# Kernel tuning notes

Measured on AMD Instinct MI355X. Metric: run time of the kernel, lower is better.

Reference implementation:

```python
import jax, jax.numpy as jnp
import numpy as np

N_HEAD = 16
COND_LEN = 256  # n_unmasked; mask[i, j] == 1 iff j < COND_LEN + i


def rotate_half(x):
    # interleaved pairs: (x0, x1, x2, x3, ...) -> (-x1, x0, -x3, x2, ...)
    x = x.reshape(x.shape[:-1] + (-1, 2))
    x1, x2 = x[..., 0], x[..., 1]
    return jnp.stack([-x2, x1], axis=-1).reshape(x.shape[:-2] + (-1,))


def apply_rotary_pos_emb(t, freqs):
    # t: [B, H, T, l], freqs: [T, l] -> broadcast over B, H
    return t * jnp.cos(freqs) + rotate_half(t) * jnp.sin(freqs)


def setup_inputs() -> dict:
    key = jax.random.key(0)
    ks = jax.random.split(key, 12)
    B, T, C = 8, 769, 1024
    l = 32
    s = 0.02
    return {
        "x_q": jax.random.normal(ks[0], (B, T, C), jnp.float32),
        "x_kv": jax.random.normal(ks[1], (B, T, C), jnp.float32),
        "rotary_pos_emb": jax.random.uniform(ks[2], (T, l), jnp.float32),
        "Wq": jax.random.normal(ks[3], (C, C), jnp.float32) * s,
        "bq": jnp.zeros((C,), jnp.float32),
        "Wk": jax.random.normal(ks[4], (C, C), jnp.float32) * s,
        "bk": jnp.zeros((C,), jnp.float32),
        "Wv": jax.random.normal(ks[5], (C, C), jnp.float32) * s,
        "bv": jnp.zeros((C,), jnp.float32),
        "Wp": jax.random.normal(ks[6], (C, C), jnp.float32) * s,
        "bp": jnp.zeros((C,), jnp.float32),
    }


def reference(x_q, x_kv, rotary_pos_emb, Wq, bq, Wk, bk, Wv, bv, Wp, bp):
    B, T_q, C = x_q.shape
    T_kv = x_kv.shape[1]
    H = N_HEAD
    hd = C // H

    def heads(x, W, b, T):
        return (x @ W.T + b).reshape(B, T, H, hd).transpose(0, 2, 1, 3)  # [B,H,T,hd]

    q = heads(x_q, Wq, bq, T_q)
    k = heads(x_kv, Wk, bk, T_kv)
    v = heads(x_kv, Wv, bv, T_kv)

    # partial rotary on first l dims of q and k
    l = rotary_pos_emb.shape[-1]
    q = jnp.concatenate([apply_rotary_pos_emb(q[..., :l], rotary_pos_emb), q[..., l:]], axis=-1)
    k = jnp.concatenate([apply_rotary_pos_emb(k[..., :l], rotary_pos_emb), k[..., l:]], axis=-1)

    att = jnp.einsum("bhqd,bhkd->bhqk", q, k) * (1.0 / jnp.sqrt(jnp.asarray(hd, q.dtype)))
    # custom prefix+causal mask: allowed iff col < COND_LEN + row
    row = jnp.arange(T_q)[:, None]
    col = jnp.arange(T_kv)[None, :]
    allowed = col < (COND_LEN + row)  # [T_q, T_kv]
    att = jnp.where(allowed[None, None], att, -jnp.inf)
    att = jax.nn.softmax(att, axis=-1)

    y = jnp.einsum("bhqk,bhkd->bhqd", att, v)
    y = y.transpose(0, 2, 1, 3).reshape(B, T_q, C)
    return y @ Wp.T + bp
```

## Files before the change

### kernel.cpp

```cpp
#include <hip/hip_runtime.h>
#include <stdint.h>

#define B_    8
#define T_    769
#define C_    1024
#define H_    16
#define COND_ 256
#define NTOK  (B_*T_)
#define BH_   (B_*H_)
#define TP_   896

typedef short    v8s  __attribute__((ext_vector_type(8)));
typedef float    v4f  __attribute__((ext_vector_type(4)));
typedef uint16_t u16x4 __attribute__((ext_vector_type(4)));
typedef uint16_t u16x8 __attribute__((ext_vector_type(8)));

__device__ __forceinline__ uint16_t f2bf(float f) {
  uint32_t u = __builtin_bit_cast(uint32_t, f);
  u += 0x7fffu + ((u >> 16) & 1u);
  return (uint16_t)(u >> 16);
}
__device__ __forceinline__ float bf2f(uint16_t h) {
  uint32_t u = ((uint32_t)h) << 16;
  return __builtin_bit_cast(float, u);
}

__device__ __forceinline__ void gl_lds16(const void* gptr, void* lptr) {
  __builtin_amdgcn_global_load_lds(
      (const __attribute__((address_space(1))) uint32_t*)gptr,
      (__attribute__((address_space(3))) uint32_t*)lptr,
      16, 0, 0);
}

__global__ __launch_bounds__(256) void convert_bf16(
    const float* xq, const float* xkv, const float* wq, const float* wk,
    const float* wv, const float* wp,
    uint16_t* dxq, uint16_t* dxkv, uint16_t* dwq, uint16_t* dwk,
    uint16_t* dwv, uint16_t* dwp)
{
  int bid = blockIdx.x;
  const float* s; uint16_t* d; int base;
  if (bid < 6152)       { s = xq;  d = dxq;  base = bid; }
  else if (bid < 12304) { s = xkv; d = dxkv; base = bid - 6152; }
  else {
    int r = bid - 12304;
    int wsel = r >> 10; base = r & 1023;
    s = (wsel == 0) ? wq : (wsel == 1) ? wk : (wsel == 2) ? wv : wp;
    d = (wsel == 0) ? dwq : (wsel == 1) ? dwk : (wsel == 2) ? dwv : dwp;
  }
  int i = base * 256 + threadIdx.x;
  float4 f = ((const float4*)s)[i];
  u16x4 o;
  o[0] = f2bf(f.x); o[1] = f2bf(f.y); o[2] = f2bf(f.z); o[3] = f2bf(f.w);
  ((u16x4*)d)[i] = o;
}

__device__ __forceinline__ void gemm_mainloop64(
    const uint16_t* A, const uint16_t* W, int M, int row0, int col0,
    v4f acc[4][4], uint16_t* sA, uint16_t* sB)
{
  const int tid = threadIdx.x;
  const int lane = tid & 63, w = tid >> 6, quad = lane >> 4, l15 = lane & 15;
  const int rbase = (w >> 1) * 64, cbase = (w & 1) * 64;

  const uint16_t* Aptr[4];
  const uint16_t* Bptr[4];
  #pragma unroll
  for (int r = 0; r < 4; r++) {
    int c = r * 256 + tid;
    int row = c >> 3, qp = c & 7;
    int g = qp ^ (row & 7);
    Aptr[r] = A + (size_t)min(row0 + row, M - 1) * 1024 + g * 8;
    Bptr[r] = W + (size_t)(col0 + row) * 1024 + g * 8;
  }

  #pragma unroll
  for (int i = 0; i < 4; i++)
    #pragma unroll
    for (int j = 0; j < 4; j++) acc[i][j] = (v4f)0.0f;

  for (int k0 = 0; k0 < 1024; k0 += 64) {
    #pragma unroll
    for (int r = 0; r < 4; r++) {
      gl_lds16(Aptr[r] + k0, sA + (r * 256 + tid) * 8);
      gl_lds16(Bptr[r] + k0, sB + (r * 256 + tid) * 8);
    }
    __syncthreads();
    #pragma unroll
    for (int s = 0; s < 2; s++) {
      v8s af[4], bf[4];
      #pragma unroll
      for (int i = 0; i < 4; i++) {
        int m = rbase + i * 16 + l15;
        af[i] = *(const v8s*)(sA + m * 64 + (((s * 4 + quad) ^ (m & 7)) * 8));
      }
      #pragma unroll
      for (int j = 0; j < 4; j++) {
        int n = cbase + j * 16 + l15;
        bf[j] = *(const v8s*)(sB + n * 64 + (((s * 4 + quad) ^ (n & 7)) * 8));
      }
      #pragma unroll
      for (int i = 0; i < 4; i++)
        #pragma unroll
        for (int j = 0; j < 4; j++)
          acc[i][j] = __builtin_amdgcn_mfma_f32_16x16x32_bf16(af[i], bf[j], acc[i][j], 0, 0, 0);
    }
    __syncthreads();
  }
}

__global__ __launch_bounds__(256) void gemm_qkv(
    const uint16_t* xq, const uint16_t* xkv, const uint16_t* Wqkv,
    const float* bq, const float* bk, const float* bv, const float* freqs,
    uint16_t* Q, uint16_t* K, uint16_t* V)
{
  __shared__ uint16_t sA[128 * 64];
  __shared__ uint16_t sB[128 * 64];
  const int ct = blockIdx.x, rt = blockIdx.y;
  const int z = ct >> 3;
  const int col0 = ct * 128, row0 = rt * 128;
  const uint16_t* A = (z == 0) ? xq : xkv;
  const float* bias  = (z == 0) ? bq : (z == 1 ? bk : bv);
  uint16_t* dst      = (z == 0) ? Q  : (z == 1 ? K  : V);

  v4f acc[4][4];
  gemm_mainloop64(A, Wqkv, NTOK, row0, col0, acc, sA, sB);

  const int tid = threadIdx.x;
  const int lane = tid & 63, w = tid >> 6, quad = lane >> 4, l15 = lane & 15;
  const int rbase = (w >> 1) * 64, cbase = (w & 1) * 64;
  #pragma unroll
  for (int i = 0; i < 4; i++) {
    #pragma unroll
    for (int reg = 0; reg < 4; reg++) {
      int n = row0 + rbase + i * 16 + quad * 4 + reg;
      bool ok = (n < NTOK);
      int nn = min(n, NTOK - 1);
      int b = nn / T_, t = nn % T_;
      float vj[4];
      #pragma unroll
      for (int j = 0; j < 4; j++)
        vj[j] = acc[i][j][reg] + bias[(col0 + cbase + j * 16 + l15) & 1023];
      if (z < 2) {
        float v0 = vj[0], v1 = vj[1];
        float p0 = __shfl_xor(v0, 1);
        float p1 = __shfl_xor(v1, 1);
        float f0 = freqs[t * 32 + l15];
        float f1 = freqs[t * 32 + 16 + l15];
        float s0, c0, s1, c1;
        __sincosf(f0, &s0, &c0);
        __sincosf(f1, &s1, &c1);
        if (l15 & 1) { vj[0] = v0 * c0 + p0 * s0; vj[1] = v1 * c1 + p1 * s1; }
        else         { vj[0] = v0 * c0 - p0 * s0; vj[1] = v1 * c1 - p1 * s1; }
      }
      if (z == 0) {
        #pragma unroll
        for (int j = 0; j < 4; j++) vj[j] *= 0.125f;
      }
      if (ok) {
        #pragma unroll
        for (int j = 0; j < 4; j++) {
          int col = col0 + cbase + j * 16 + l15;
          int h = (col >> 6) & 15, d = col & 63;
          dst[((size_t)(b * H_ + h) * T_ + t) * 64 + d] = f2bf(vj[j]);
        }
      }
    }
  }
}

__global__ __launch_bounds__(256) void gemm_out(
    const uint16_t* Y, const uint16_t* wp, const float* bp, float* out)
{
  __shared__ uint16_t sA[128 * 64];
  __shared__ uint16_t sB[128 * 64];
  const int col0 = blockIdx.x * 128, row0 = blockIdx.y * 128;
  v4f acc[4][4];
  gemm_mainloop64(Y, wp, NTOK, row0, col0, acc, sA, sB);

  const int tid = threadIdx.x;
  const int lane = tid & 63, w = tid >> 6, quad = lane >> 4, l15 = lane & 15;
  const int rbase = (w >> 1) * 64, cbase = (w & 1) * 64;
  #pragma unroll
  for (int i = 0; i < 4; i++) {
    #pragma unroll
    for (int reg = 0; reg < 4; reg++) {
      int n = row0 + rbase + i * 16 + quad * 4 + reg;
      if (n < NTOK) {
        #pragma unroll
        for (int j = 0; j < 4; j++) {
          int col = col0 + cbase + j * 16 + l15;
          out[(size_t)n * 1024 + col] = acc[i][j][reg] + bp[col];
        }
      }
    }
  }
}

__global__ __launch_bounds__(256) void transpose_v(const uint16_t* Vb, uint16_t* Vt)
{
  __shared__ uint16_t sT[64 * 64];
  const int tid = threadIdx.x;
  const int t0 = blockIdx.x * 64, bh = blockIdx.y;
  const uint16_t* src = Vb + (size_t)bh * T_ * 64;
  #pragma unroll
  for (int r = 0; r < 2; r++) {
    int task = r * 256 + tid;
    int t = task >> 3, oc = task & 7;
    int gt = min(t0 + t, T_ - 1);
    u16x8 v = *(const u16x8*)(src + (size_t)gt * 64 + oc * 8);
    int p = oc ^ (t & 7) ^ ((t >> 3) & 7);
    *(u16x8*)(sT + t * 64 + p * 8) = v;
  }
  __syncthreads();
  uint16_t* dst = Vt + (size_t)bh * 64 * TP_;
  #pragma unroll
  for (int r = 0; r < 2; r++) {
    int task = r * 256 + tid;
    int o = task & 7, d = task >> 3;
    u16x8 v;
    #pragma unroll
    for (int k = 0; k < 8; k++) {
      int t = o * 8 + k;
      int p = (d >> 3) ^ k ^ o;
      v[k] = sT[t * 64 + p * 8 + (d & 7)];
    }
    *(u16x8*)(dst + (size_t)d * TP_ + t0 + o * 8) = v;
  }
}

__global__ __launch_bounds__(256) void attn(
    const uint16_t* Q, const uint16_t* K, const uint16_t* Vt, uint16_t* Y)
{
  __shared__ uint16_t sK[128 * 64];
  __shared__ uint16_t sVT[64 * 128];
  __shared__ uint16_t sP[4 * 16 * 136];

  const int tid = threadIdx.x;
  const int lane = tid & 63, w = tid >> 6, quad = lane >> 4, l15 = lane & 15;
  const int bh = blockIdx.y, b = bh >> 4, h = bh & 15;
  const int q0 = blockIdx.x * 64;

  const uint16_t* Qb = Q + (size_t)bh * T_ * 64;
  const uint16_t* Kb = K + (size_t)bh * T_ * 64;
  const uint16_t* Vtb = Vt + (size_t)bh * 64 * TP_;

  const int qr = min(q0 + w * 16 + l15, T_ - 1);
  v8s aq0 = *(const v8s*)(Qb + (size_t)qr * 64 + quad * 8);
  v8s aq1 = *(const v8s*)(Qb + (size_t)qr * 64 + 32 + quad * 8);

  float l_r[4] = {0.f, 0.f, 0.f, 0.f};
  v4f o[4];
  #pragma unroll
  for (int r = 0; r < 4; r++) o[r] = (v4f)0.0f;

  const int kend = min(T_, q0 + 319);
  const int nkt = (kend + 127) >> 7;

  for (int kt = 0; kt < nkt; kt++) {
    const int k0 = kt * 128;
    #pragma unroll
    for (int r = 0; r < 4; r++) {
      int c = r * 256 + tid;
      int key = c >> 3, qp = c & 7;
      int g = qp ^ (key & 7);
      int gk = min(k0 + key, T_ - 1);
      gl_lds16(Kb + (size_t)gk * 64 + g * 8, sK + c * 8);
    }
    #pragma unroll
    for (int r = 0; r < 4; r++) {
      int c = r * 256 + tid;
      int d = c >> 4, p = c & 15;
      int g = (p & 8) | ((p ^ d) & 7);
      gl_lds16(Vtb + (size_t)d * TP_ + k0 + g * 8, sVT + c * 8);
    }
    __syncthreads();

    v4f s[8];
    #pragma unroll
    for (int cb = 0; cb < 8; cb++) {
      int key_l = cb * 16 + l15;
      v8s b0 = *(const v8s*)(sK + (key_l * 8 + ((quad) ^ (key_l & 7))) * 8);
      v8s b1 = *(const v8s*)(sK + (key_l * 8 + ((4 + quad) ^ (key_l & 7))) * 8);
      v4f zz = (v4f)0.0f;
      zz = __builtin_amdgcn_mfma_f32_16x16x32_bf16(aq0, b0, zz, 0, 0, 0);
      zz = __builtin_amdgcn_mfma_f32_16x16x32_bf16(aq1, b1, zz, 0, 0, 0);
      s[cb] = zz;
    }

    uint16_t* pw = sP + w * (16 * 136);
    const int qrow_base = q0 + w * 16 + quad * 4;
    const bool full = (k0 + 128 <= COND_ + q0) && (k0 + 128 <= T_);
    if (full) {
      #pragma unroll
      for (int reg = 0; reg < 4; reg++) {
        float rs = 0.f;
        #pragma unroll
        for (int cb = 0; cb < 8; cb++) {
          float pv = __expf(s[cb][reg]);
          uint16_t pb = f2bf(pv);
          rs += bf2f(pb);
          pw[(quad * 4 + reg) * 136 + cb * 16 + l15] = pb;
        }
        #pragma unroll
        for (int off = 1; off < 16; off <<= 1) rs += __shfl_xor(rs, off);
        l_r[reg] += rs;
      }
    } else {
      #pragma unroll
      for (int reg = 0; reg < 4; reg++) {
        int lim = min(COND_ + qrow_base + reg, T_);
        float rs = 0.f;
        #pragma unroll
        for (int cb = 0; cb < 8; cb++) {
          int key = k0 + cb * 16 + l15;
          float pv = (key < lim) ? __expf(s[cb][reg]) : 0.f;
          uint16_t pb = f2bf(pv);
          rs += bf2f(pb);
          pw[(quad * 4 + reg) * 136 + cb * 16 + l15] = pb;
        }
        #pragma unroll
        for (int off = 1; off < 16; off <<= 1) rs += __shfl_xor(rs, off);
        l_r[reg] += rs;
      }
    }

    #pragma unroll
    for (int ks = 0; ks < 4; ks++) {
      v8s ap = *(const v8s*)(pw + l15 * 136 + ks * 32 + quad * 8);
      #pragma unroll
      for (int cbd = 0; cbd < 4; cbd++) {
        int d = cbd * 16 + l15;
        v8s bv = *(const v8s*)(sVT + d * 128 + (((ks * 4 + quad) ^ (d & 7)) * 8));
        o[cbd] = __builtin_amdgcn_mfma_f32_16x16x32_bf16(ap, bv, o[cbd], 0, 0, 0);
      }
    }
    __syncthreads();
  }

  #pragma unroll
  for (int reg = 0; reg < 4; reg++) {
    int t = q0 + w * 16 + quad * 4 + reg;
    if (t < T_) {
      float inv = 1.0f / l_r[reg];
      #pragma unroll
      for (int cbd = 0; cbd < 4; cbd++) {
        int d = cbd * 16 + l15;
        Y[((size_t)(b * T_ + t)) * C_ + h * 64 + d] = f2bf(o[cbd][reg] * inv);
      }
    }
  }
}

extern "C" void kernel_launch(void* const* d_in, const int* in_sizes, int n_in,
                              void* d_out, int out_size, void* d_ws, size_t ws_size,
                              hipStream_t stream)
{
  const float* x_q   = (const float*)d_in[0];
  const float* x_kv  = (const float*)d_in[1];
  const float* freqs = (const float*)d_in[2];
  const float* Wq = (const float*)d_in[3];
  const float* bq = (const float*)d_in[4];
  const float* Wk = (const float*)d_in[5];
  const float* bk = (const float*)d_in[6];
  const float* Wv = (const float*)d_in[7];
  const float* bv = (const float*)d_in[8];
  const float* Wp = (const float*)d_in[9];
  const float* bp = (const float*)d_in[10];
  float* out = (float*)d_out;

  const size_t SZX = (size_t)NTOK * C_;
  const size_t SZW = (size_t)C_ * C_;
  uint16_t* ws = (uint16_t*)d_ws;
  uint16_t* xq_bf  = ws;
  uint16_t* xkv_bf = xq_bf + SZX;
  uint16_t* wq_bf  = xkv_bf + SZX;
  uint16_t* wk_bf  = wq_bf + SZW;
  uint16_t* wv_bf  = wk_bf + SZW;
  uint16_t* wp_bf  = wv_bf + SZW;
  uint16_t* Qb = wp_bf + SZW;
  uint16_t* Kb = Qb + SZX;
  uint16_t* Vb = Kb + SZX;
  uint16_t* Vt = ws;
  uint16_t* Yb = Vb;

  convert_bf16<<<dim3(16400), 256, 0, stream>>>(
      x_q, x_kv, Wq, Wk, Wv, Wp, xq_bf, xkv_bf, wq_bf, wk_bf, wv_bf, wp_bf);

  gemm_qkv<<<dim3(24, 49), 256, 0, stream>>>(
      xq_bf, xkv_bf, wq_bf, bq, bk, bv, freqs, Qb, Kb, Vb);

  transpose_v<<<dim3(13, BH_), 256, 0, stream>>>(Vb, Vt);

  attn<<<dim3(13, BH_), 256, 0, stream>>>(Qb, Kb, Vt, Yb);

  gemm_out<<<dim3(8, 49), 256, 0, stream>>>(Yb, wp_bf, bp, out);
}
```

Before: 279.7 us.

## Load GEMM A operand directly from global memory, stage only weights in LDS

The GEMM mainloop stops staging the activation tile in shared memory. Each lane now reads its A fragments straight from global memory into registers, while the weight tile is staged with a K-step of 128 and a new swizzle. This removes the A-side LDS traffic and halves the number of barriers per K sweep. The cost is uncoalesced-ish 16-byte global loads per lane, with the two warps that share rows fetching the same A data twice, and the global load latency is now exposed directly in the MFMA loop.

```diff
diff --git a/kernel.cpp b/kernel.cpp
--- a/kernel.cpp
+++ b/kernel.cpp
@@ -55,22 +55,25 @@
   ((u16x4*)d)[i] = o;
 }
 
-__device__ __forceinline__ void gemm_mainloop64(
+__device__ __forceinline__ void gemm_mainloop_ad(
     const uint16_t* A, const uint16_t* W, int M, int row0, int col0,
-    v4f acc[4][4], uint16_t* sA, uint16_t* sB)
+    v4f acc[4][4], uint16_t* sB)
 {
   const int tid = threadIdx.x;
   const int lane = tid & 63, w = tid >> 6, quad = lane >> 4, l15 = lane & 15;
   const int rbase = (w >> 1) * 64, cbase = (w & 1) * 64;
 
-  const uint16_t* Aptr[4];
-  const uint16_t* Bptr[4];
-  #pragma unroll
-  for (int r = 0; r < 4; r++) {
+  const uint16_t* Arow[4];
+  #pragma unroll
+  for (int i = 0; i < 4; i++)
+    Arow[i] = A + (size_t)min(row0 + rbase + i * 16 + l15, M - 1) * 1024 + quad * 8;
+
+  const uint16_t* Bptr[8];
+  #pragma unroll
+  for (int r = 0; r < 8; r++) {
     int c = r * 256 + tid;
-    int row = c >> 3, qp = c & 7;
-    int g = qp ^ (row & 7);
-    Aptr[r] = A + (size_t)min(row0 + row, M - 1) * 1024 + g * 8;
+    int row = c >> 4, p = c & 15;
+    int g = (p & 8) | ((p ^ row) & 7);
     Bptr[r] = W + (size_t)(col0 + row) * 1024 + g * 8;
   }
 
@@ -79,25 +82,23 @@
     #pragma unroll
     for (int j = 0; j < 4; j++) acc[i][j] = (v4f)0.0f;
 
-  for (int k0 = 0; k0 < 1024; k0 += 64) {
-    #pragma unroll
-    for (int r = 0; r < 4; r++) {
-      gl_lds16(Aptr[r] + k0, sA + (r * 256 + tid) * 8);
+  for (int k0 = 0; k0 < 1024; k0 += 128) {
+    #pragma unroll
+    for (int r = 0; r < 8; r++)
       gl_lds16(Bptr[r] + k0, sB + (r * 256 + tid) * 8);
-    }
     __syncthreads();
     #pragma unroll
-    for (int s = 0; s < 2; s++) {
+    for (int ks = 0; ks < 4; ks++) {
       v8s af[4], bf[4];
       #pragma unroll
-      for (int i = 0; i < 4; i++) {
-        int m = rbase + i * 16 + l15;
-        af[i] = *(const v8s*)(sA + m * 64 + (((s * 4 + quad) ^ (m & 7)) * 8));
-      }
+      for (int i = 0; i < 4; i++)
+        af[i] = *(const v8s*)(Arow[i] + k0 + ks * 32);
+      const int q = ks * 4 + quad;
       #pragma unroll
       for (int j = 0; j < 4; j++) {
         int n = cbase + j * 16 + l15;
-        bf[j] = *(const v8s*)(sB + n * 64 + (((s * 4 + quad) ^ (n & 7)) * 8));
+        int p = (q & 8) | ((q ^ n) & 7);
+        bf[j] = *(const v8s*)(sB + n * 128 + p * 8);
       }
       #pragma unroll
       for (int i = 0; i < 4; i++)
@@ -114,8 +115,7 @@
     const float* bq, const float* bk, const float* bv, const float* freqs,
     uint16_t* Q, uint16_t* K, uint16_t* V)
 {
-  __shared__ uint16_t sA[128 * 64];
-  __shared__ uint16_t sB[128 * 64];
+  __shared__ uint16_t sB[128 * 128];
   const int ct = blockIdx.x, rt = blockIdx.y;
   const int z = ct >> 3;
   const int col0 = ct * 128, row0 = rt * 128;
@@ -124,7 +124,7 @@
   uint16_t* dst      = (z == 0) ? Q  : (z == 1 ? K  : V);
 
   v4f acc[4][4];
-  gemm_mainloop64(A, Wqkv, NTOK, row0, col0, acc, sA, sB);
+  gemm_mainloop_ad(A, Wqkv, NTOK, row0, col0, acc, sB);
 
   const int tid = threadIdx.x;
   const int lane = tid & 63, w = tid >> 6, quad = lane >> 4, l15 = lane & 15;
@@ -172,11 +172,10 @@
 __global__ __launch_bounds__(256) void gemm_out(
     const uint16_t* Y, const uint16_t* wp, const float* bp, float* out)
 {
-  __shared__ uint16_t sA[128 * 64];
-  __shared__ uint16_t sB[128 * 64];
+  __shared__ uint16_t sB[128 * 128];
   const int col0 = blockIdx.x * 128, row0 = blockIdx.y * 128;
   v4f acc[4][4];
-  gemm_mainloop64(Y, wp, NTOK, row0, col0, acc, sA, sB);
+  gemm_mainloop_ad(Y, wp, NTOK, row0, col0, acc, sB);
 
   const int tid = threadIdx.x;
   const int lane = tid & 63, w = tid >> 6, quad = lane >> 4, l15 = lane & 15;
```

Result: slower. 346.0 us (+23.7%).

## Process 128 queries per attention block to reuse K/V tiles

Applied to the files above, without the earlier changes.

Each attention block now covers 128 query rows instead of 64, with every wave handling two 16-row subtiles. Each K/V tile staged in LDS therefore serves twice as many queries, roughly halving global K/V traffic and barrier count per query. The grid shrinks from 13 to 7 blocks per head. The trade-offs are more registers per thread (two accumulator sets), coarser work units, and more padded wasted work in the final tile, since the last block holds only one valid query row.

```diff
diff --git a/kernel.cpp b/kernel.cpp
--- a/kernel.cpp
+++ b/kernel.cpp
@@ -239,22 +239,29 @@
   const int tid = threadIdx.x;
   const int lane = tid & 63, w = tid >> 6, quad = lane >> 4, l15 = lane & 15;
   const int bh = blockIdx.y, b = bh >> 4, h = bh & 15;
-  const int q0 = blockIdx.x * 64;
+  const int q0 = blockIdx.x * 128;
+  const int qw = q0 + w * 32;
 
   const uint16_t* Qb = Q + (size_t)bh * T_ * 64;
   const uint16_t* Kb = K + (size_t)bh * T_ * 64;
   const uint16_t* Vtb = Vt + (size_t)bh * 64 * TP_;
 
-  const int qr = min(q0 + w * 16 + l15, T_ - 1);
-  v8s aq0 = *(const v8s*)(Qb + (size_t)qr * 64 + quad * 8);
-  v8s aq1 = *(const v8s*)(Qb + (size_t)qr * 64 + 32 + quad * 8);
-
-  float l_r[4] = {0.f, 0.f, 0.f, 0.f};
-  v4f o[4];
-  #pragma unroll
-  for (int r = 0; r < 4; r++) o[r] = (v4f)0.0f;
-
-  const int kend = min(T_, q0 + 319);
+  v8s aq[2][2];
+  #pragma unroll
+  for (int i = 0; i < 2; i++) {
+    int qr = min(qw + i * 16 + l15, T_ - 1);
+    aq[i][0] = *(const v8s*)(Qb + (size_t)qr * 64 + quad * 8);
+    aq[i][1] = *(const v8s*)(Qb + (size_t)qr * 64 + 32 + quad * 8);
+  }
+
+  float l_r[2][4];
+  v4f o[2][4];
+  #pragma unroll
+  for (int i = 0; i < 2; i++)
+    #pragma unroll
+    for (int r = 0; r < 4; r++) { l_r[i][r] = 0.f; o[i][r] = (v4f)0.0f; }
+
+  const int kend = min(T_, COND_ + q0 + 127);
   const int nkt = (kend + 127) >> 7;
 
   for (int kt = 0; kt < nkt; kt++) {
@@ -276,77 +283,83 @@
     }
     __syncthreads();
 
-    v4f s[8];
-    #pragma unroll
-    for (int cb = 0; cb < 8; cb++) {
-      int key_l = cb * 16 + l15;
-      v8s b0 = *(const v8s*)(sK + (key_l * 8 + ((quad) ^ (key_l & 7))) * 8);
-      v8s b1 = *(const v8s*)(sK + (key_l * 8 + ((4 + quad) ^ (key_l & 7))) * 8);
-      v4f zz = (v4f)0.0f;
-      zz = __builtin_amdgcn_mfma_f32_16x16x32_bf16(aq0, b0, zz, 0, 0, 0);
-      zz = __builtin_amdgcn_mfma_f32_16x16x32_bf16(aq1, b1, zz, 0, 0, 0);
-      s[cb] = zz;
-    }
-
     uint16_t* pw = sP + w * (16 * 136);
-    const int qrow_base = q0 + w * 16 + quad * 4;
-    const bool full = (k0 + 128 <= COND_ + q0) && (k0 + 128 <= T_);
-    if (full) {
-      #pragma unroll
-      for (int reg = 0; reg < 4; reg++) {
-        float rs = 0.f;
-        #pragma unroll
-        for (int cb = 0; cb < 8; cb++) {
-          float pv = __expf(s[cb][reg]);
-          uint16_t pb = f2bf(pv);
-          rs += bf2f(pb);
-          pw[(quad * 4 + reg) * 136 + cb * 16 + l15] = pb;
-        }
-        #pragma unroll
-        for (int off = 1; off < 16; off <<= 1) rs += __shfl_xor(rs, off);
-        l_r[reg] += rs;
-      }
-    } else {
-      #pragma unroll
-      for (int reg = 0; reg < 4; reg++) {
-        int lim = min(COND_ + qrow_base + reg, T_);
-        float rs = 0.f;
-        #pragma unroll
-        for (int cb = 0; cb < 8; cb++) {
-          int key = k0 + cb * 16 + l15;
-          float pv = (key < lim) ? __expf(s[cb][reg]) : 0.f;
-          uint16_t pb = f2bf(pv);
-          rs += bf2f(pb);
-          pw[(quad * 4 + reg) * 136 + cb * 16 + l15] = pb;
-        }
-        #pragma unroll
-        for (int off = 1; off < 16; off <<= 1) rs += __shfl_xor(rs, off);
-        l_r[reg] += rs;
-      }
-    }
-
-    #pragma unroll
-    for (int ks = 0; ks < 4; ks++) {
-      v8s ap = *(const v8s*)(pw + l15 * 136 + ks * 32 + quad * 8);
-      #pragma unroll
-      for (int cbd = 0; cbd < 4; cbd++) {
-        int d = cbd * 16 + l15;
-        v8s bv = *(const v8s*)(sVT + d * 128 + (((ks * 4 + quad) ^ (d & 7)) * 8));
-        o[cbd] = __builtin_amdgcn_mfma_f32_16x16x32_bf16(ap, bv, o[cbd], 0, 0, 0);
+    #pragma unroll
+    for (int i = 0; i < 2; i++) {
+      v4f s[8];
+      #pragma unroll
+      for (int cb = 0; cb < 8; cb++) {
+        int key_l = cb * 16 + l15;
+        v8s b0 = *(const v8s*)(sK + (key_l * 8 + ((quad) ^ (key_l & 7))) * 8);
+        v8s b1 = *(const v8s*)(sK + (key_l * 8 + ((4 + quad) ^ (key_l & 7))) * 8);
+        v4f zz = (v4f)0.0f;
+        zz = __builtin_amdgcn_mfma_f32_16x16x32_bf16(aq[i][0], b0, zz, 0, 0, 0);
+        zz = __builtin_amdgcn_mfma_f32_16x16x32_bf16(aq[i][1], b1, zz, 0, 0, 0);
+        s[cb] = zz;
+      }
+
+      const int rowb = qw + i * 16 + quad * 4;
+      const bool full = (k0 + 128 <= COND_ + qw + i * 16) && (k0 + 128 <= T_);
+      if (full) {
+        #pragma unroll
+        for (int reg = 0; reg < 4; reg++) {
+          float rs = 0.f;
+          #pragma unroll
+          for (int cb = 0; cb < 8; cb++) {
+            float pv = __expf(s[cb][reg]);
+            uint16_t pb = f2bf(pv);
+            rs += bf2f(pb);
+            pw[(quad * 4 + reg) * 136 + cb * 16 + l15] = pb;
+          }
+          #pragma unroll
+          for (int off = 1; off < 16; off <<= 1) rs += __shfl_xor(rs, off);
+          l_r[i][reg] += rs;
+        }
+      } else {
+        #pragma unroll
+        for (int reg = 0; reg < 4; reg++) {
+          int lim = min(COND_ + rowb + reg, T_);
+          float rs = 0.f;
+          #pragma unroll
+          for (int cb = 0; cb < 8; cb++) {
+            int key = k0 + cb * 16 + l15;
+            float pv = (key < lim) ? __expf(s[cb][reg]) : 0.f;
+            uint16_t pb = f2bf(pv);
+            rs += bf2f(pb);
+            pw[(quad * 4 + reg) * 136 + cb * 16 + l15] = pb;
+          }
+          #pragma unroll
+          for (int off = 1; off < 16; off <<= 1) rs += __shfl_xor(rs, off);
+          l_r[i][reg] += rs;
+        }
+      }
+
+      #pragma unroll
+      for (int ks = 0; ks < 4; ks++) {
+        v8s ap = *(const v8s*)(pw + l15 * 136 + ks * 32 + quad * 8);
+        #pragma unroll
+        for (int cbd = 0; cbd < 4; cbd++) {
+          int d = cbd * 16 + l15;
+          v8s bv = *(const v8s*)(sVT + d * 128 + (((ks * 4 + quad) ^ (d & 7)) * 8));
+          o[i][cbd] = __builtin_amdgcn_mfma_f32_16x16x32_bf16(ap, bv, o[i][cbd], 0, 0, 0);
+        }
       }
     }
     __syncthreads();
   }
 
   #pragma unroll
-  for (int reg = 0; reg < 4; reg++) {
-    int t = q0 + w * 16 + quad * 4 + reg;
-    if (t < T_) {
-      float inv = 1.0f / l_r[reg];
-      #pragma unroll
-      for (int cbd = 0; cbd < 4; cbd++) {
-        int d = cbd * 16 + l15;
-        Y[((size_t)(b * T_ + t)) * C_ + h * 64 + d] = f2bf(o[cbd][reg] * inv);
+  for (int i = 0; i < 2; i++) {
+    #pragma unroll
+    for (int reg = 0; reg < 4; reg++) {
+      int t = qw + i * 16 + quad * 4 + reg;
+      if (t < T_) {
+        float inv = 1.0f / l_r[i][reg];
+        #pragma unroll
+        for (int cbd = 0; cbd < 4; cbd++) {
+          int d = cbd * 16 + l15;
+          Y[((size_t)(b * T_ + t)) * C_ + h * 64 + d] = f2bf(o[i][cbd][reg] * inv);
+        }
       }
     }
   }
@@ -392,7 +405,7 @@
 
   transpose_v<<<dim3(13, BH_), 256, 0, stream>>>(Vb, Vt);
 
-  attn<<<dim3(13, BH_), 256, 0, stream>>>(Qb, Kb, Vt, Yb);
+  attn<<<dim3(7, BH_), 256, 0, stream>>>(Qb, Kb, Vt, Yb);
 
   gemm_out<<<dim3(8, 49), 256, 0, stream>>>(Yb, wp_bf, bp, out);
 }
```

New measurement: 291.9 us. 1.04x slower.

## Permute key order in P/V so probabilities pack into vector stores; MFMA row sums

Applied to the files above, without the earlier changes.

The attention kernel now writes each lane's 8 bf16 probabilities as one 128-bit LDS store instead of 8 scalar stores. This permutes the key order inside each 128-key tile. The V transpose kernel is rewritten with 128-token tiles to lay out V^T in the matching permuted order. Softmax row sums now come from an extra MFMA against a ones vector, replacing the per-row shuffle reductions. This trades shuffle and scalar-store work for one extra MFMA per k-step and couples the two kernels' layouts.

```diff
diff --git a/kernel.cpp b/kernel.cpp
--- a/kernel.cpp
+++ b/kernel.cpp
@@ -14,15 +14,12 @@
 typedef float    v4f  __attribute__((ext_vector_type(4)));
 typedef uint16_t u16x4 __attribute__((ext_vector_type(4)));
 typedef uint16_t u16x8 __attribute__((ext_vector_type(8)));
+typedef uint32_t u32x4 __attribute__((ext_vector_type(4)));
 
 __device__ __forceinline__ uint16_t f2bf(float f) {
   uint32_t u = __builtin_bit_cast(uint32_t, f);
   u += 0x7fffu + ((u >> 16) & 1u);
   return (uint16_t)(u >> 16);
-}
-__device__ __forceinline__ float bf2f(uint16_t h) {
-  uint32_t u = ((uint32_t)h) << 16;
-  return __builtin_bit_cast(float, u);
 }
 
 __device__ __forceinline__ void gl_lds16(const void* gptr, void* lptr) {
@@ -199,33 +196,30 @@
 
 __global__ __launch_bounds__(256) void transpose_v(const uint16_t* Vb, uint16_t* Vt)
 {
-  __shared__ uint16_t sT[64 * 64];
-  const int tid = threadIdx.x;
-  const int t0 = blockIdx.x * 64, bh = blockIdx.y;
+  __shared__ uint16_t sT[128 * 64];
+  const int tid = threadIdx.x;
+  const int t0 = blockIdx.x * 128, bh = blockIdx.y;
   const uint16_t* src = Vb + (size_t)bh * T_ * 64;
   #pragma unroll
-  for (int r = 0; r < 2; r++) {
+  for (int r = 0; r < 4; r++) {
     int task = r * 256 + tid;
     int t = task >> 3, oc = task & 7;
     int gt = min(t0 + t, T_ - 1);
     u16x8 v = *(const u16x8*)(src + (size_t)gt * 64 + oc * 8);
-    int p = oc ^ (t & 7) ^ ((t >> 3) & 7);
-    *(u16x8*)(sT + t * 64 + p * 8) = v;
+    *(u16x8*)(sT + t * 64 + ((oc ^ (t & 7)) * 8)) = v;
   }
   __syncthreads();
   uint16_t* dst = Vt + (size_t)bh * 64 * TP_;
   #pragma unroll
-  for (int r = 0; r < 2; r++) {
-    int task = r * 256 + tid;
-    int o = task & 7, d = task >> 3;
+  for (int r = 0; r < 4; r++) {
+    int d = tid & 63, c = (tid >> 6) + r * 4;
     u16x8 v;
     #pragma unroll
-    for (int k = 0; k < 8; k++) {
-      int t = o * 8 + k;
-      int p = (d >> 3) ^ k ^ o;
-      v[k] = sT[t * 64 + p * 8 + (d & 7)];
-    }
-    *(u16x8*)(dst + (size_t)d * TP_ + t0 + o * 8) = v;
+    for (int j = 0; j < 8; j++) {
+      int t = j * 16 + c;
+      v[j] = sT[t * 64 + (((d >> 3) ^ (t & 7)) * 8) + (d & 7)];
+    }
+    *(u16x8*)(dst + (size_t)d * TP_ + t0 + c * 8) = v;
   }
 }
 
@@ -249,7 +243,11 @@
   v8s aq0 = *(const v8s*)(Qb + (size_t)qr * 64 + quad * 8);
   v8s aq1 = *(const v8s*)(Qb + (size_t)qr * 64 + 32 + quad * 8);
 
-  float l_r[4] = {0.f, 0.f, 0.f, 0.f};
+  v8s vones;
+  #pragma unroll
+  for (int j = 0; j < 8; j++) vones[j] = (short)0x3F80;
+
+  v4f lacc = (v4f)0.0f;
   v4f o[4];
   #pragma unroll
   for (int r = 0; r < 4; r++) o[r] = (v4f)0.0f;
@@ -289,45 +287,33 @@
     }
 
     uint16_t* pw = sP + w * (16 * 136);
-    const int qrow_base = q0 + w * 16 + quad * 4;
     const bool full = (k0 + 128 <= COND_ + q0) && (k0 + 128 <= T_);
-    if (full) {
-      #pragma unroll
-      for (int reg = 0; reg < 4; reg++) {
-        float rs = 0.f;
-        #pragma unroll
-        for (int cb = 0; cb < 8; cb++) {
-          float pv = __expf(s[cb][reg]);
-          uint16_t pb = f2bf(pv);
-          rs += bf2f(pb);
-          pw[(quad * 4 + reg) * 136 + cb * 16 + l15] = pb;
-        }
-        #pragma unroll
-        for (int off = 1; off < 16; off <<= 1) rs += __shfl_xor(rs, off);
-        l_r[reg] += rs;
-      }
-    } else {
-      #pragma unroll
-      for (int reg = 0; reg < 4; reg++) {
-        int lim = min(COND_ + qrow_base + reg, T_);
-        float rs = 0.f;
+    #pragma unroll
+    for (int reg = 0; reg < 4; reg++) {
+      const int lr = quad * 4 + reg;
+      float pv[8];
+      if (full) {
+        #pragma unroll
+        for (int cb = 0; cb < 8; cb++) pv[cb] = __expf(s[cb][reg]);
+      } else {
+        int lim = min(COND_ + q0 + w * 16 + lr, T_);
         #pragma unroll
         for (int cb = 0; cb < 8; cb++) {
           int key = k0 + cb * 16 + l15;
-          float pv = (key < lim) ? __expf(s[cb][reg]) : 0.f;
-          uint16_t pb = f2bf(pv);
-          rs += bf2f(pb);
-          pw[(quad * 4 + reg) * 136 + cb * 16 + l15] = pb;
+          pv[cb] = (key < lim) ? __expf(s[cb][reg]) : 0.f;
         }
-        #pragma unroll
-        for (int off = 1; off < 16; off <<= 1) rs += __shfl_xor(rs, off);
-        l_r[reg] += rs;
-      }
+      }
+      u32x4 pk;
+      #pragma unroll
+      for (int cc = 0; cc < 4; cc++)
+        pk[cc] = (uint32_t)f2bf(pv[2 * cc]) | ((uint32_t)f2bf(pv[2 * cc + 1]) << 16);
+      *(u32x4*)(pw + lr * 136 + l15 * 8) = pk;
     }
 
     #pragma unroll
     for (int ks = 0; ks < 4; ks++) {
-      v8s ap = *(const v8s*)(pw + l15 * 136 + ks * 32 + quad * 8);
+      v8s ap = *(const v8s*)(pw + l15 * 136 + (ks * 4 + quad) * 8);
+      lacc = __builtin_amdgcn_mfma_f32_16x16x32_bf16(ap, vones, lacc, 0, 0, 0);
       #pragma unroll
       for (int cbd = 0; cbd < 4; cbd++) {
         int d = cbd * 16 + l15;
@@ -342,7 +328,7 @@
   for (int reg = 0; reg < 4; reg++) {
     int t = q0 + w * 16 + quad * 4 + reg;
     if (t < T_) {
-      float inv = 1.0f / l_r[reg];
+      float inv = 1.0f / lacc[reg];
       #pragma unroll
       for (int cbd = 0; cbd < 4; cbd++) {
         int d = cbd * 16 + l15;
@@ -390,7 +376,7 @@
   gemm_qkv<<<dim3(24, 49), 256, 0, stream>>>(
       xq_bf, xkv_bf, wq_bf, bq, bk, bv, freqs, Qb, Kb, Vb);
 
-  transpose_v<<<dim3(13, BH_), 256, 0, stream>>>(Vb, Vt);
+  transpose_v<<<dim3(7, BH_), 256, 0, stream>>>(Vb, Vt);
 
   attn<<<dim3(13, BH_), 256, 0, stream>>>(Qb, Kb, Vt, Yb);
 
```

After: 280.8 us. No clear change (+0.4%).
